# Optimization experiments

Measured on AMD Instinct MI355X. Metric: run time of the kernel, lower is better.

The kernel has to match this reference:

```python
import jax, jax.numpy as jnp
import numpy as np

NUM_HEADS = 12

def setup_inputs() -> dict:
    key = jax.random.key(0)
    ks = jax.random.split(key, 8)
    B, N, C, H, R = 8, 1024, 768, NUM_HEADS, 4
    hd = C // H
    x = jax.random.normal(ks[0], (B, N, C), dtype=jnp.float32)
    Wqkv = jax.random.normal(ks[1], (3 * C, C), dtype=jnp.float32) * (C ** -0.5)
    Wproj = jax.random.normal(ks[2], (C, C), dtype=jnp.float32) * (C ** -0.5)
    bproj = jnp.zeros((C,), dtype=jnp.float32)
    Aq = jax.random.normal(ks[3], (hd, R), dtype=jnp.float32) * (hd ** -0.5)
    Bq = jax.random.normal(ks[4], (R, hd), dtype=jnp.float32) * (R ** -0.5)
    Av = jax.random.normal(ks[5], (hd, R), dtype=jnp.float32) * (hd ** -0.5)
    Bv = jax.random.normal(ks[6], (R, hd), dtype=jnp.float32) * (R ** -0.5)
    return {"x": x, "Wqkv": Wqkv, "Wproj": Wproj, "bproj": bproj,
            "Aq": Aq, "Bq": Bq, "Av": Av, "Bv": Bv}

def reference(x, Wqkv, Wproj, bproj, Aq, Bq, Av, Bv):
    B, N, C = x.shape
    H = NUM_HEADS
    hd = C // H
    scale = hd ** -0.5
    # QKV projection: [B,N,3C] -> [3,B,H,N,hd]
    qkv = (x @ Wqkv.T).reshape(B, N, 3, H, hd).transpose(2, 0, 3, 1, 4)
    q, k, v = qkv[0], qkv[1], qkv[2]
    # LoRA low-rank deltas on Q and V
    q = q + (q @ Aq) @ Bq
    v = v + (v @ Av) @ Bv
    # Attention scores [B,H,N,N]
    attn = jnp.einsum('bhnd,bhmd->bhnm', q, k) * scale
    attn = jax.nn.softmax(attn, axis=-1)
    out = jnp.einsum('bhnm,bhmd->bhnd', attn, v)  # [B,H,N,hd]
    out = out.transpose(0, 2, 1, 3).reshape(B, N, C)
    return out @ Wproj.T + bproj
```

## Files before the change

kernel.cpp:

```cpp
#include <hip/hip_runtime.h>

#define DEV __device__ __forceinline__

typedef _Float16 f16x8 __attribute__((ext_vector_type(8)));
typedef _Float16 f16x4 __attribute__((ext_vector_type(4)));
typedef float f32x4 __attribute__((ext_vector_type(4)));
typedef float f32x16 __attribute__((ext_vector_type(16)));
typedef unsigned int u32x4 __attribute__((ext_vector_type(4)));
typedef unsigned int u32x2 __attribute__((ext_vector_type(2)));

DEV void glds16(const void* g, void* l) {
    __builtin_amdgcn_global_load_lds(
        (const __attribute__((address_space(1))) void*)g,
        (__attribute__((address_space(3))) void*)l, 16, 0, 0);
}

DEV unsigned pkh(float lo, float hi) {
    return __builtin_bit_cast(unsigned, __builtin_amdgcn_cvt_pkrtz(lo, hi));
}

__global__ __launch_bounds__(256) void cast_f32_f16(const float* __restrict__ src,
                                                    _Float16* __restrict__ dst, int n4) {
    const int i = blockIdx.x * 256 + threadIdx.x;
    if (i >= n4) return;
    const float4 v = ((const float4*)src)[i];
    f16x4 o = { (_Float16)v.x, (_Float16)v.y, (_Float16)v.z, (_Float16)v.w };
    *(f16x4*)(dst + (size_t)i * 4) = o;
}

__global__ __launch_bounds__(256) void prep_w(const float* __restrict__ W,
                                              const float* __restrict__ Aq,
                                              const float* __restrict__ Bq,
                                              const float* __restrict__ Av,
                                              const float* __restrict__ Bv,
                                              _Float16* __restrict__ Wb) {
    const int bx = blockIdx.x;
    const int sec = bx / 12;
    const int h = bx - sec * 12;
    const float* Am = sec ? Av : Aq;
    const float* Bm = sec ? Bv : Bq;
    const int base = sec ? (1536 + h * 64) : (h * 64);
    const float scale = sec ? 1.0f : (0.125f * 1.4426950408889634f);
    const int c = blockIdx.y * 256 + threadIdx.x;
    float t0 = 0.f, t1 = 0.f, t2 = 0.f, t3 = 0.f;
    for (int j = 0; j < 64; ++j) {
        const float w = W[(size_t)(base + j) * 768 + c];
        t0 += Am[j * 4 + 0] * w;
        t1 += Am[j * 4 + 1] * w;
        t2 += Am[j * 4 + 2] * w;
        t3 += Am[j * 4 + 3] * w;
    }
    for (int i = 0; i < 64; ++i) {
        const float w = W[(size_t)(base + i) * 768 + c];
        const float val = w + t0 * Bm[i] + t1 * Bm[64 + i] + t2 * Bm[128 + i] + t3 * Bm[192 + i];
        Wb[(size_t)(base + i) * 768 + c] = (_Float16)(val * scale);
    }
}

template <int EPI, int MF, int GX, int GY>
__global__ __launch_bounds__(256) void gemm_nt(const _Float16* __restrict__ A,
                                               const _Float16* __restrict__ B,
                                               int Kdim, void* __restrict__ Cout,
                                               const float* __restrict__ bias) {
    constexpr int BM = MF * 32;
    constexpr int XB = GX / 8;
    __shared__ __align__(16) _Float16 As[BM * 64];
    __shared__ __align__(16) _Float16 Bs[128 * 64];
    const int tid = threadIdx.x;
    const int lane = tid & 63, wid = tid >> 6;
    const int l15 = lane & 15, l16 = lane >> 4;
    const int id = blockIdx.x;
    const int xcd = id & 7, c = id >> 3;
    const int bx = xcd * XB + (c % XB), by = c / XB;
    const int m0 = bx * BM, n0 = by << 7;
    const int wm = (wid >> 1) * (MF * 16), wn = (wid & 1) << 6;

    auto stage = [&](int k0) {
#pragma unroll
        for (int rr = 0; rr < MF; ++rr) {
            const int slot = (rr << 8) + tid;
            const int row = slot >> 3, sl = slot & 7;
            glds16(A + (size_t)(m0 + row) * Kdim + k0 + ((sl ^ (row & 7)) << 3),
                   (char*)As + (((rr << 8) + (wid << 6)) << 4));
        }
#pragma unroll
        for (int rr = 0; rr < 4; ++rr) {
            const int slot = (rr << 8) + tid;
            const int row = slot >> 3, sl = slot & 7;
            glds16(B + (size_t)(n0 + row) * Kdim + k0 + ((sl ^ (row & 7)) << 3),
                   (char*)Bs + (((rr << 8) + (wid << 6)) << 4));
        }
    };

    f32x4 acc[MF][4];
#pragma unroll
    for (int i = 0; i < MF; ++i)
#pragma unroll
        for (int j = 0; j < 4; ++j) acc[i][j] = (f32x4){0.f, 0.f, 0.f, 0.f};

    stage(0);
    __syncthreads();

    for (int k0 = 0; k0 < Kdim; k0 += 64) {
        f16x8 af[2][MF], bf[2][4];
#pragma unroll
        for (int kh = 0; kh < 2; ++kh) {
#pragma unroll
            for (int i = 0; i < MF; ++i) {
                const int ra = wm + i * 16 + l15;
                af[kh][i] = *(const f16x8*)((const char*)As + ra * 128 +
                                            ((((kh << 2) + l16) ^ (ra & 7)) << 4));
            }
#pragma unroll
            for (int j = 0; j < 4; ++j) {
                const int rb = wn + j * 16 + l15;
                bf[kh][j] = *(const f16x8*)((const char*)Bs + rb * 128 +
                                            ((((kh << 2) + l16) ^ (rb & 7)) << 4));
            }
        }
        __syncthreads();
        if (k0 + 64 < Kdim) stage(k0 + 64);
        __builtin_amdgcn_sched_barrier(0);
#pragma unroll
        for (int kh = 0; kh < 2; ++kh)
#pragma unroll
            for (int i = 0; i < MF; ++i)
#pragma unroll
                for (int j = 0; j < 4; ++j)
                    acc[i][j] = __builtin_amdgcn_mfma_f32_16x16x32_f16(af[kh][i], bf[kh][j],
                                                                       acc[i][j], 0, 0, 0);
        __syncthreads();
    }

    if (EPI == 0) {
        _Float16* qkv = (_Float16*)Cout;
#pragma unroll
        for (int j = 0; j < 4; ++j) {
            const int col = n0 + wn + j * 16 + l15;
            const int which = col / 768;
            const int rem = col - which * 768;
            const int hh = rem >> 6, d = rem & 63;
#pragma unroll
            for (int i = 0; i < MF; ++i) {
                const int rowb = m0 + wm + i * 16 + (l16 << 2);
                const int b = rowb >> 10, n = rowb & 1023;
                const int b12h = b * 12 + hh;
                if (which == 2) {
                    f16x4 pk = { (_Float16)acc[i][j][0], (_Float16)acc[i][j][1],
                                 (_Float16)acc[i][j][2], (_Float16)acc[i][j][3] };
                    *(f16x4*)(qkv + 12582912 +
                              ((((size_t)b12h * 64 + (n >> 4)) * 64 + d) << 4) + (n & 15)) = pk;
                } else if (which == 1) {
                    const size_t hb = 6291456 + ((size_t)b12h << 16);
#pragma unroll
                    for (int r = 0; r < 4; ++r) {
                        const int kv = n + r;
                        const int off = ((((kv >> 5) << 2) + (d >> 4)) << 9) +
                                        ((((kv & 31) << 1) + ((d >> 3) & 1)) << 3) + (d & 7);
                        qkv[hb + off] = (_Float16)acc[i][j][r];
                    }
                } else {
#pragma unroll
                    for (int r = 0; r < 4; ++r)
                        qkv[(((size_t)b12h << 10) + n + r) * 64 + d] = (_Float16)acc[i][j][r];
                }
            }
        }
    } else {
        float* out = (float*)Cout;
#pragma unroll
        for (int j = 0; j < 4; ++j) {
            const int col = n0 + wn + j * 16 + l15;
            const float bv = bias[col];
#pragma unroll
            for (int i = 0; i < MF; ++i)
#pragma unroll
                for (int r = 0; r < 4; ++r) {
                    const int row = m0 + wm + i * 16 + (l16 << 2) + r;
                    out[(size_t)row * 768 + col] = acc[i][j][r] + bv;
                }
        }
    }
}

__global__ __launch_bounds__(512) void attn_kernel(const _Float16* __restrict__ Qg,
                                                   const _Float16* __restrict__ K4g,
                                                   const _Float16* __restrict__ V4g,
                                                   _Float16* __restrict__ AO) {
    __shared__ float lds_o[4][64][32];
    __shared__ float2 lds_ml[4][32];

    const int tid = threadIdx.x, lane = tid & 63, wid = tid >> 6;
    const int l31 = lane & 31, hi = lane >> 5;
    const int wq = wid & 3, kvhalf = wid >> 2;
    const int bh = blockIdx.x;
    const int q = (blockIdx.y << 7) + (wq << 5) + l31;
    const int tbase = kvhalf << 4;
    const _Float16* K4h = K4g + ((size_t)bh << 16);
    const _Float16* V4h = V4g + ((size_t)bh << 16);

    f16x8 qf[4];
#pragma unroll
    for (int kd = 0; kd < 4; ++kd)
        qf[kd] = *(const f16x8*)(Qg + (((size_t)bh << 10) + q) * 64 + kd * 16 + hi * 8);

    f32x16 o0, o1;
#pragma unroll
    for (int j = 0; j < 16; ++j) { o0[j] = 0.f; o1[j] = 0.f; }
    float m_run = -INFINITY, l_run = 0.f;

    f16x8 kf[4], vf[4];
    f32x16 st;

#pragma unroll
    for (int kd = 0; kd < 4; ++kd)
        kf[kd] = *(const f16x8*)(K4h + ((size_t)((tbase << 2) + kd) << 9) +
                                 (((l31 << 1) + hi) << 3));
#pragma unroll
    for (int j = 0; j < 16; ++j) st[j] = 0.f;
#pragma unroll
    for (int kd = 0; kd < 4; ++kd)
        st = __builtin_amdgcn_mfma_f32_32x32x16_f16(kf[kd], qf[kd], st, 0, 0, 0);
#pragma unroll
    for (int kd = 0; kd < 4; ++kd)
        kf[kd] = *(const f16x8*)(K4h + ((size_t)(((tbase + 1) << 2) + kd) << 9) +
                                 (((l31 << 1) + hi) << 3));

#pragma unroll 1
    for (int kt = 0; kt < 16; ++kt) {
        const int tt = tbase + kt;

#pragma unroll
        for (int dh = 0; dh < 2; ++dh)
#pragma unroll
            for (int ks = 0; ks < 2; ++ks)
                vf[dh * 2 + ks] = *(const f16x8*)(V4h + ((size_t)((tt << 1) + ks) << 10) +
                                                  ((dh * 32 + l31) << 4) + hi * 8);

        float tr[8];
#pragma unroll
        for (int j = 0; j < 8; ++j) tr[j] = fmaxf(st[2 * j], st[2 * j + 1]);
#pragma unroll
        for (int j = 0; j < 4; ++j) tr[j] = fmaxf(tr[j], tr[j + 4]);
        float mx = fmaxf(fmaxf(tr[0], tr[2]), fmaxf(tr[1], tr[3]));
        mx = fmaxf(mx, __shfl_xor(mx, 32));
        if (!__all(mx <= m_run + 8.f)) {
            const float mnew = fmaxf(m_run, mx);
            const float fac = __builtin_amdgcn_exp2f(m_run - mnew);
            l_run *= fac;
#pragma unroll
            for (int j = 0; j < 16; ++j) { o0[j] *= fac; o1[j] *= fac; }
            m_run = mnew;
        }
#pragma unroll
        for (int j = 0; j < 16; ++j) st[j] = __builtin_amdgcn_exp2f(st[j] - m_run);
        float sr[8];
#pragma unroll
        for (int j = 0; j < 8; ++j) sr[j] = st[2 * j] + st[2 * j + 1];
#pragma unroll
        for (int j = 0; j < 4; ++j) sr[j] = sr[j] + sr[j + 4];
        l_run += (sr[0] + sr[2]) + (sr[1] + sr[3]);

        const unsigned a0 = pkh(st[0], st[1]),   a1 = pkh(st[2], st[3]);
        const unsigned a2 = pkh(st[4], st[5]),   a3 = pkh(st[6], st[7]);
        const unsigned a4 = pkh(st[8], st[9]),   a5 = pkh(st[10], st[11]);
        const unsigned a6 = pkh(st[12], st[13]), a7 = pkh(st[14], st[15]);
        const unsigned s0 = (unsigned)__shfl_xor((int)(hi ? a0 : a2), 32);
        const unsigned s1 = (unsigned)__shfl_xor((int)(hi ? a1 : a3), 32);
        const unsigned s2 = (unsigned)__shfl_xor((int)(hi ? a4 : a6), 32);
        const unsigned s3 = (unsigned)__shfl_xor((int)(hi ? a5 : a7), 32);

#pragma unroll
        for (int j = 0; j < 16; ++j) st[j] = 0.f;
#pragma unroll
        for (int kd = 0; kd < 4; ++kd)
            st = __builtin_amdgcn_mfma_f32_32x32x16_f16(kf[kd], qf[kd], st, 0, 0, 0);

        const int tn = tbase + ((kt + 2) & 15);
#pragma unroll
        for (int kd = 0; kd < 4; ++kd)
            kf[kd] = *(const f16x8*)(K4h + ((size_t)((tn << 2) + kd) << 9) +
                                     (((l31 << 1) + hi) << 3));
        __builtin_amdgcn_sched_barrier(0);

        const u32x4 w0 = { hi ? s0 : a0, hi ? s1 : a1, hi ? a2 : s0, hi ? a3 : s1 };
        const u32x4 w1 = { hi ? s2 : a4, hi ? s3 : a5, hi ? a6 : s2, hi ? a7 : s3 };
        const f16x8 pa0 = __builtin_bit_cast(f16x8, w0);
        const f16x8 pa1 = __builtin_bit_cast(f16x8, w1);

        o0 = __builtin_amdgcn_mfma_f32_32x32x16_f16(vf[0], pa0, o0, 0, 0, 0);
        o0 = __builtin_amdgcn_mfma_f32_32x32x16_f16(vf[1], pa1, o0, 0, 0, 0);
        o1 = __builtin_amdgcn_mfma_f32_32x32x16_f16(vf[2], pa0, o1, 0, 0, 0);
        o1 = __builtin_amdgcn_mfma_f32_32x32x16_f16(vf[3], pa1, o1, 0, 0, 0);
    }

    l_run += __shfl_xor(l_run, 32);

    if (kvhalf) {
#pragma unroll
        for (int g = 0; g < 4; ++g) {
            *(f32x4*)&lds_o[wq][lane][4 * g] =
                (f32x4){o0[4 * g + 0], o0[4 * g + 1], o0[4 * g + 2], o0[4 * g + 3]};
            *(f32x4*)&lds_o[wq][lane][16 + 4 * g] =
                (f32x4){o1[4 * g + 0], o1[4 * g + 1], o1[4 * g + 2], o1[4 * g + 3]};
        }
        if (!hi) lds_ml[wq][l31] = make_float2(m_run, l_run);
    }
    __syncthreads();
    if (kvhalf) return;

    const float2 ml2 = lds_ml[wq][l31];
    const float M = fmaxf(m_run, ml2.x);
    const float f1 = __builtin_amdgcn_exp2f(m_run - M);
    const float f2 = __builtin_amdgcn_exp2f(ml2.x - M);
    const float inv = __builtin_amdgcn_rcpf(l_run * f1 + ml2.y * f2);
    const float c1 = f1 * inv, c2 = f2 * inv;

    const int b = bh / 12, h = bh - (bh / 12) * 12;
    _Float16* dst = AO + ((size_t)b * 1024 + q) * 768 + h * 64 + hi * 4;
#pragma unroll
    for (int g = 0; g < 4; ++g) {
        const f32x4 p0 = *(const f32x4*)&lds_o[wq][lane][4 * g];
        const f32x4 p1 = *(const f32x4*)&lds_o[wq][lane][16 + 4 * g];
        const u32x2 w0 = { pkh(o0[4 * g + 0] * c1 + p0[0] * c2, o0[4 * g + 1] * c1 + p0[1] * c2),
                           pkh(o0[4 * g + 2] * c1 + p0[2] * c2, o0[4 * g + 3] * c1 + p0[3] * c2) };
        *(f16x4*)(dst + g * 8) = __builtin_bit_cast(f16x4, w0);
        const u32x2 w1 = { pkh(o1[4 * g + 0] * c1 + p1[0] * c2, o1[4 * g + 1] * c1 + p1[1] * c2),
                           pkh(o1[4 * g + 2] * c1 + p1[2] * c2, o1[4 * g + 3] * c1 + p1[3] * c2) };
        *(f16x4*)(dst + 32 + g * 8) = __builtin_bit_cast(f16x4, w1);
    }
}

extern "C" void kernel_launch(void* const* d_in, const int* in_sizes, int n_in,
                              void* d_out, int out_size, void* d_ws, size_t ws_size,
                              hipStream_t stream) {
    (void)in_sizes; (void)n_in; (void)out_size; (void)ws_size;
    const float* x     = (const float*)d_in[0];
    const float* Wqkv  = (const float*)d_in[1];
    const float* Wproj = (const float*)d_in[2];
    const float* bproj = (const float*)d_in[3];
    const float* Aq    = (const float*)d_in[4];
    const float* Bq    = (const float*)d_in[5];
    const float* Av    = (const float*)d_in[6];
    const float* Bv    = (const float*)d_in[7];

    _Float16* Xb     = (_Float16*)d_ws;
    _Float16* Wqkvb  = Xb + 6291456;
    _Float16* Wprojb = Wqkvb + 1769472;
    _Float16* QKV    = Wprojb + 589824;
    _Float16* AO     = QKV + 18874368;
    float* out = (float*)d_out;

    cast_f32_f16<<<6144, 256, 0, stream>>>(x, Xb, 1572864);
    cast_f32_f16<<<576, 256, 0, stream>>>(Wqkv + 589824, Wqkvb + 589824, 147456);
    cast_f32_f16<<<576, 256, 0, stream>>>(Wproj, Wprojb, 147456);
    prep_w<<<dim3(24, 3), 256, 0, stream>>>(Wqkv, Aq, Bq, Av, Bv, Wqkvb);

    gemm_nt<0, 4, 64, 18><<<1152, 256, 0, stream>>>(Xb, Wqkvb, 768, (void*)QKV, nullptr);
    attn_kernel<<<dim3(96, 8), 512, 0, stream>>>(QKV, QKV + 6291456, QKV + 12582912, AO);
    gemm_nt<1, 2, 128, 6><<<768, 256, 0, stream>>>(AO, Wprojb, 768, (void*)out, bproj);
}
```

Before: 121.7 us.

## Merge prep kernels into one launch and add MFMA priority hints in attention

The three cast kernels and the LoRA weight-folding kernel become one launch, prep_all, which dispatches on block index to remove three launch gaps. The LoRA blocks sit at the lowest block indices so the slow serial weight work starts first. In the attention loop, the row-max reduction is restructured into grouped fmax triples, and s_setprio(1)/s_setprio(0) is placed around the MFMA groups to favour matrix-issue waves. The merged kernel mixes divergent block types, and the priority hints may have little effect.

```diff
diff --git a/kernel.cpp b/kernel.cpp
--- a/kernel.cpp
+++ b/kernel.cpp
@@ -19,42 +19,57 @@
     return __builtin_bit_cast(unsigned, __builtin_amdgcn_cvt_pkrtz(lo, hi));
 }
 
-__global__ __launch_bounds__(256) void cast_f32_f16(const float* __restrict__ src,
-                                                    _Float16* __restrict__ dst, int n4) {
-    const int i = blockIdx.x * 256 + threadIdx.x;
-    if (i >= n4) return;
+__global__ __launch_bounds__(256) void prep_all(const float* __restrict__ x,
+                                                const float* __restrict__ Wqkv,
+                                                const float* __restrict__ Wproj,
+                                                const float* __restrict__ Aq,
+                                                const float* __restrict__ Bq,
+                                                const float* __restrict__ Av,
+                                                const float* __restrict__ Bv,
+                                                _Float16* __restrict__ Xb,
+                                                _Float16* __restrict__ Wqkvb,
+                                                _Float16* __restrict__ Wprojb) {
+    const int blk = blockIdx.x;
+    if (blk < 72) {
+        const int bx = blk % 24, cy = blk / 24;
+        const int sec = bx / 12;
+        const int h = bx - sec * 12;
+        const float* Am = sec ? Av : Aq;
+        const float* Bm = sec ? Bv : Bq;
+        const int base = sec ? (1536 + h * 64) : (h * 64);
+        const float scale = sec ? 1.0f : (0.125f * 1.4426950408889634f);
+        const int c = cy * 256 + threadIdx.x;
+        float t0 = 0.f, t1 = 0.f, t2 = 0.f, t3 = 0.f;
+        for (int j = 0; j < 64; ++j) {
+            const float w = Wqkv[(size_t)(base + j) * 768 + c];
+            t0 += Am[j * 4 + 0] * w;
+            t1 += Am[j * 4 + 1] * w;
+            t2 += Am[j * 4 + 2] * w;
+            t3 += Am[j * 4 + 3] * w;
+        }
+        for (int i = 0; i < 64; ++i) {
+            const float w = Wqkv[(size_t)(base + i) * 768 + c];
+            const float val = w + t0 * Bm[i] + t1 * Bm[64 + i] + t2 * Bm[128 + i] + t3 * Bm[192 + i];
+            Wqkvb[(size_t)(base + i) * 768 + c] = (_Float16)(val * scale);
+        }
+        return;
+    }
+    const float* src;
+    _Float16* dst;
+    int i;
+    if (blk < 6216) {
+        i = (blk - 72) * 256 + threadIdx.x;
+        src = x; dst = Xb;
+    } else if (blk < 6792) {
+        i = (blk - 6216) * 256 + threadIdx.x;
+        src = Wqkv + 589824; dst = Wqkvb + 589824;
+    } else {
+        i = (blk - 6792) * 256 + threadIdx.x;
+        src = Wproj; dst = Wprojb;
+    }
     const float4 v = ((const float4*)src)[i];
     f16x4 o = { (_Float16)v.x, (_Float16)v.y, (_Float16)v.z, (_Float16)v.w };
     *(f16x4*)(dst + (size_t)i * 4) = o;
-}
-
-__global__ __launch_bounds__(256) void prep_w(const float* __restrict__ W,
-                                              const float* __restrict__ Aq,
-                                              const float* __restrict__ Bq,
-                                              const float* __restrict__ Av,
-                                              const float* __restrict__ Bv,
-                                              _Float16* __restrict__ Wb) {
-    const int bx = blockIdx.x;
-    const int sec = bx / 12;
-    const int h = bx - sec * 12;
-    const float* Am = sec ? Av : Aq;
-    const float* Bm = sec ? Bv : Bq;
-    const int base = sec ? (1536 + h * 64) : (h * 64);
-    const float scale = sec ? 1.0f : (0.125f * 1.4426950408889634f);
-    const int c = blockIdx.y * 256 + threadIdx.x;
-    float t0 = 0.f, t1 = 0.f, t2 = 0.f, t3 = 0.f;
-    for (int j = 0; j < 64; ++j) {
-        const float w = W[(size_t)(base + j) * 768 + c];
-        t0 += Am[j * 4 + 0] * w;
-        t1 += Am[j * 4 + 1] * w;
-        t2 += Am[j * 4 + 2] * w;
-        t3 += Am[j * 4 + 3] * w;
-    }
-    for (int i = 0; i < 64; ++i) {
-        const float w = W[(size_t)(base + i) * 768 + c];
-        const float val = w + t0 * Bm[i] + t1 * Bm[64 + i] + t2 * Bm[128 + i] + t3 * Bm[192 + i];
-        Wb[(size_t)(base + i) * 768 + c] = (_Float16)(val * scale);
-    }
 }
 
 template <int EPI, int MF, int GX, int GY>
@@ -237,12 +252,12 @@
                 vf[dh * 2 + ks] = *(const f16x8*)(V4h + ((size_t)((tt << 1) + ks) << 10) +
                                                   ((dh * 32 + l31) << 4) + hi * 8);
 
-        float tr[8];
-#pragma unroll
-        for (int j = 0; j < 8; ++j) tr[j] = fmaxf(st[2 * j], st[2 * j + 1]);
-#pragma unroll
-        for (int j = 0; j < 4; ++j) tr[j] = fmaxf(tr[j], tr[j + 4]);
-        float mx = fmaxf(fmaxf(tr[0], tr[2]), fmaxf(tr[1], tr[3]));
+        const float g0 = fmaxf(fmaxf(st[0], st[1]), st[2]);
+        const float g1 = fmaxf(fmaxf(st[3], st[4]), st[5]);
+        const float g2 = fmaxf(fmaxf(st[6], st[7]), st[8]);
+        const float g3 = fmaxf(fmaxf(st[9], st[10]), st[11]);
+        const float g4 = fmaxf(fmaxf(st[12], st[13]), st[14]);
+        float mx = fmaxf(fmaxf(fmaxf(g0, g1), g2), fmaxf(fmaxf(g3, g4), st[15]));
         mx = fmaxf(mx, __shfl_xor(mx, 32));
         if (!__all(mx <= m_run + 8.f)) {
             const float mnew = fmaxf(m_run, mx);
@@ -272,9 +287,11 @@
 
 #pragma unroll
         for (int j = 0; j < 16; ++j) st[j] = 0.f;
+        __builtin_amdgcn_s_setprio(1);
 #pragma unroll
         for (int kd = 0; kd < 4; ++kd)
             st = __builtin_amdgcn_mfma_f32_32x32x16_f16(kf[kd], qf[kd], st, 0, 0, 0);
+        __builtin_amdgcn_s_setprio(0);
 
         const int tn = tbase + ((kt + 2) & 15);
 #pragma unroll
@@ -288,10 +305,12 @@
         const f16x8 pa0 = __builtin_bit_cast(f16x8, w0);
         const f16x8 pa1 = __builtin_bit_cast(f16x8, w1);
 
+        __builtin_amdgcn_s_setprio(1);
         o0 = __builtin_amdgcn_mfma_f32_32x32x16_f16(vf[0], pa0, o0, 0, 0, 0);
         o0 = __builtin_amdgcn_mfma_f32_32x32x16_f16(vf[1], pa1, o0, 0, 0, 0);
         o1 = __builtin_amdgcn_mfma_f32_32x32x16_f16(vf[2], pa0, o1, 0, 0, 0);
         o1 = __builtin_amdgcn_mfma_f32_32x32x16_f16(vf[3], pa1, o1, 0, 0, 0);
+        __builtin_amdgcn_s_setprio(0);
     }
 
     l_run += __shfl_xor(l_run, 32);
@@ -351,10 +370,8 @@
     _Float16* AO     = QKV + 18874368;
     float* out = (float*)d_out;
 
-    cast_f32_f16<<<6144, 256, 0, stream>>>(x, Xb, 1572864);
-    cast_f32_f16<<<576, 256, 0, stream>>>(Wqkv + 589824, Wqkvb + 589824, 147456);
-    cast_f32_f16<<<576, 256, 0, stream>>>(Wproj, Wprojb, 147456);
-    prep_w<<<dim3(24, 3), 256, 0, stream>>>(Wqkv, Aq, Bq, Av, Bv, Wqkvb);
+    prep_all<<<7368, 256, 0, stream>>>(x, Wqkv, Wproj, Aq, Bq, Av, Bv,
+                                       Xb, Wqkvb, Wprojb);
 
     gemm_nt<0, 4, 64, 18><<<1152, 256, 0, stream>>>(Xb, Wqkvb, 768, (void*)QKV, nullptr);
     attn_kernel<<<dim3(96, 8), 512, 0, stream>>>(QKV, QKV + 6291456, QKV + 12582912, AO);
```

Result: faster. 114.4 us (-6.0%).
